# Optimization experiments

Measured on AMD Instinct MI355X. Metric: run time of the kernel, lower is better.

The kernel has to match this reference:

```python
import jax, jax.numpy as jnp
import numpy as np

N, E = 50000, 500000
IN, C, CE_IN = 128, 64, 16   # raw node dim, mid_channel, raw edge dim
L = 3                        # num_layers: layer0 = bare conv, layers 1..2 = res+ blocks
LN_EPS = 1e-5


def layer_norm(x, g, b):
    mu = x.mean(-1, keepdims=True)
    var = ((x - mu) ** 2).mean(-1, keepdims=True)
    return (x - mu) * jax.lax.rsqrt(var + LN_EPS) * g + b


def sage_conv(x, e, src, dst, W1, b1, W2, b2, Wr, t):
    """SAGEConvV2 with softmax aggregation. Returns (node_out, per-edge messages)."""
    # message: lin_l(cat([x_i, x_j, edge_attr])) ; x_i = dst (target), x_j = src (source)
    m_in = jnp.concatenate([x[dst], x[src], e], axis=-1)          # [E, 2C+Ce]
    m = jax.nn.relu(m_in @ W1 + b1) @ W2 + b2                      # [E, C]
    # scatter_softmax(m * t, dst) per feature channel
    logits = m * t
    seg_max = jax.ops.segment_max(logits, dst, num_segments=N)    # [N, C]
    w = jnp.exp(logits - seg_max[dst])
    w = w / jax.ops.segment_sum(w, dst, num_segments=N)[dst]
    out = jax.ops.segment_sum(m * w, dst, num_segments=N)         # [N, C]
    out = out + x @ Wr                                             # root weight (no bias)
    return out, m


def setup_inputs() -> dict:
    key = jax.random.key(0)
    ks = jax.random.split(key, 18)
    f32 = jnp.float32

    def w(k, shape, fan_in):
        return (jax.random.normal(k, shape, f32) / np.sqrt(fan_in)).astype(f32)

    inp = {
        "x": jax.random.normal(ks[0], (N, IN), f32),
        "edge_index": jax.random.randint(ks[1], (2, E), 0, N, dtype=jnp.int64),
        "edge_attr": jax.random.normal(ks[2], (E, CE_IN), f32),
        # encoders
        "node_W": w(ks[3], (IN, C), IN),
        "node_b": jnp.zeros((C,), f32),
        "edge_W": w(ks[4], (CE_IN, C), CE_IN),
        "edge_b": jnp.zeros((C,), f32),
        # stacked conv params (L convs, identical shapes)
        "conv_W1": w(ks[5], (L, 3 * C, 2 * C), 3 * C),
        "conv_b1": jnp.zeros((L, 2 * C), f32),
        "conv_W2": w(ks[6], (L, 2 * C, C), 2 * C),
        "conv_b2": jnp.zeros((L, C), f32),
        "conv_Wr": w(ks[7], (L, C, C), C),
        "conv_t": jnp.ones((L,), f32),
        # layer norms: ln_g[0]/ln_b[0] used as the final output norm, 1..2 inside res+ blocks
        "ln_g": jnp.ones((L, C), f32),
        "ln_b": jnp.zeros((L, C), f32),
        "eln_g": jnp.ones((L - 1, C), f32),
        "eln_b": jnp.zeros((L - 1, C), f32),
    }
    return inp


def reference(x, edge_index, edge_attr, node_W, node_b, edge_W, edge_b,
              conv_W1, conv_b1, conv_W2, conv_b2, conv_Wr, conv_t,
              ln_g, ln_b, eln_g, eln_b):
    src, dst = edge_index[0], edge_index[1]
    h = x @ node_W + node_b                    # node encoder
    e = edge_attr @ edge_W + edge_b            # edge encoder
    # first layer: bare conv
    h, e = sage_conv(h, e, src, dst, conv_W1[0], conv_b1[0], conv_W2[0],
                     conv_b2[0], conv_Wr[0], conv_t[0])
    # res+ blocks (dropout is identity in eval mode)
    for i in range(1, L):
        hn = jax.nn.relu(layer_norm(h, ln_g[i], ln_b[i]))
        en = layer_norm(e, eln_g[i - 1], eln_b[i - 1])
        dh, m = sage_conv(hn, en, src, dst, conv_W1[i], conv_b1[i], conv_W2[i],
                          conv_b2[i], conv_Wr[i], conv_t[i])
        h = h + dh
        e = e + m
    # final norm + act (uses layer-0 norm params, as in the canonical DeeperGCN example)
    return jax.nn.relu(layer_norm(h, ln_g[0], ln_b[0]))
```

## Files before the change

### kernel.cpp

```cpp
#include <hip/hip_runtime.h>

typedef unsigned short u16;
typedef unsigned int u32;
typedef __attribute__((ext_vector_type(8))) short short8;
typedef __attribute__((ext_vector_type(4))) float floatx4;

#define LN_EPS 1e-5f

__device__ __forceinline__ float bf2f(u16 u) {
    union { u32 i; float f; } v; v.i = ((u32)u) << 16; return v.f;
}
__device__ __forceinline__ u16 f2bf(float f) {
    union { u32 i; float f; } v; v.f = f;
    u32 x = v.i;
    return (u16)((x + 0x7fffu + ((x >> 16) & 1u)) >> 16);
}
__device__ __forceinline__ int clampi(int v, int lo, int hi) {
    return v < lo ? lo : (v > hi ? hi : v);
}

__device__ __forceinline__ void g2lds16(const void* g, void* l) {
    __builtin_amdgcn_global_load_lds(
        (__attribute__((address_space(1))) const u32*)g,
        (__attribute__((address_space(3))) u32*)l, 16, 0, 0);
}

__global__ void k_fill(float* __restrict__ out, int nel, float val) {
    int i = blockIdx.x * blockDim.x + threadIdx.x;
    if (i < nel) out[i] = val;
}

__global__ void k_pre0(const int* __restrict__ ei, int E, int* __restrict__ flag,
                       int* __restrict__ deg, int n,
                       const float* __restrict__ W1, const float* __restrict__ W2,
                       const float* __restrict__ Wr, const float* __restrict__ nW,
                       u16* __restrict__ W1s, u16* __restrict__ W2s,
                       u16* __restrict__ Wrs, u16* __restrict__ nWs) {
    int t = threadIdx.x;
    if (blockIdx.x == 0) {
        __shared__ int any;
        if (t == 0) any = 0;
        __syncthreads();
        int lim = (E < 4096) ? E : 4096;
        int v = 0;
        for (int i = t; i < lim; i += 256) v |= ei[2 * i + 1];
        if (v) atomicOr(&any, 1);
        __syncthreads();
        if (t == 0) flag[0] = (any == 0) ? 1 : 0;
    }
    int i = blockIdx.x * 256 + t;
    if (i < n) deg[i] = 0;
    if (i < 3 * 24576) {
        int l = i / 24576, rem = i % 24576;
        int k = rem / 128, c = rem % 128;
        int kt = k >> 5, q = (k >> 3) & 3, j = k & 7;
        W1s[l * 24576 + ((kt * 4 + q) * 128 + c) * 8 + j] = f2bf(W1[i]);
    }
    if (i < 3 * 8192) {
        int l = i / 8192, rem = i % 8192;
        int k = rem / 64, c = rem % 64;
        int kt = k >> 5, q = (k >> 3) & 3, j = k & 7;
        W2s[l * 8192 + ((kt * 4 + q) * 64 + c) * 8 + j] = f2bf(W2[i]);
    }
    if (i < 3 * 4096) {
        int l = i / 4096, rem = i % 4096;
        int k = rem / 64, c = rem % 64;
        int kt = k >> 5, q = (k >> 3) & 3, j = k & 7;
        Wrs[l * 4096 + ((kt * 4 + q) * 64 + c) * 8 + j] = f2bf(Wr[i]);
    }
    if (i < 8192) {
        int k = i / 64, c = i % 64;
        int kt = k >> 5, q = (k >> 3) & 3, j = k & 7;
        nWs[((kt * 4 + q) * 64 + c) * 8 + j] = f2bf(nW[i]);
    }
}

__global__ void k_hist(const int* __restrict__ ei, const int* __restrict__ flag,
                       int* __restrict__ deg, int E, int n) {
    int e = blockIdx.x * blockDim.x + threadIdx.x;
    if (e < E) {
        int d = flag[0] ? ei[2 * ((size_t)E + e)] : ei[(size_t)E + e];
        atomicAdd(&deg[clampi(d, 0, n - 1)], 1);
    }
}

__global__ void k_scan1(const int* __restrict__ deg, int* __restrict__ offs,
                        int* __restrict__ bsum, int n) {
    __shared__ int s[256];
    int t = threadIdx.x;
    int i = blockIdx.x * 256 + t;
    int v = (i < n) ? deg[i] : 0;
    s[t] = v; __syncthreads();
    for (int off = 1; off < 256; off <<= 1) {
        int x = (t >= off) ? s[t - off] : 0;
        __syncthreads();
        s[t] += x;
        __syncthreads();
    }
    if (i < n) offs[i] = s[t] - v;
    if (t == 255) bsum[blockIdx.x] = s[255];
}

__global__ void k_scan23(int* __restrict__ offs, const int* __restrict__ bsum,
                         int* __restrict__ cursor, int n, int E, int nb) {
    __shared__ int s[256];
    int t = threadIdx.x;
    int v = (t < nb) ? bsum[t] : 0;
    s[t] = v; __syncthreads();
    for (int off = 1; off < 256; off <<= 1) {
        int x = (t >= off) ? s[t - off] : 0;
        __syncthreads();
        s[t] += x;
        __syncthreads();
    }
    int excl = s[blockIdx.x] - bsum[blockIdx.x];
    int i = blockIdx.x * 256 + t;
    if (i < n) {
        int val = offs[i] + excl;
        offs[i] = val;
        cursor[i] = val;
    }
    if (i == 0) offs[n] = E;
}

__global__ void k_scatter(const int* __restrict__ ei, const int* __restrict__ flag,
                          int* __restrict__ cursor,
                          int* __restrict__ perm, int* __restrict__ srcs,
                          int* __restrict__ dsts, int E, int n) {
    int e = blockIdx.x * blockDim.x + threadIdx.x;
    if (e < E) {
        int sv, dv;
        if (flag[0]) {
            sv = ei[2 * (size_t)e];
            dv = ei[2 * ((size_t)E + e)];
        } else {
            sv = ei[e];
            dv = ei[(size_t)E + e];
        }
        sv = clampi(sv, 0, n - 1);
        dv = clampi(dv, 0, n - 1);
        int p = clampi(atomicAdd(&cursor[dv], 1), 0, E - 1);
        perm[p] = e;
        srcs[p] = sv;
        dsts[p] = dv;
    }
}

#define HSTR 136

__global__ __launch_bounds__(512) void k_enc(
    const float* __restrict__ x, const u16* __restrict__ nWs, const float* __restrict__ nbias,
    const u16* __restrict__ Wrs0,
    float* __restrict__ h, u16* __restrict__ hn, int n,
    const float* __restrict__ ea, const int* __restrict__ perm,
    const float* __restrict__ eW, const float* __restrict__ ebias,
    u16* __restrict__ e_s, int E, int RB) {
    __shared__ __align__(16) short sA[8 * 16 * HSTR];
    int t = threadIdx.x;
    if ((int)blockIdx.x < RB) {
        int w = t >> 6, l = t & 63, q = l >> 4, ml = l & 15;
        int wbase = blockIdx.x * 128 + w * 16;
        int rin = wbase + ml;
        int rr = (rin < n) ? rin : 0;
        const float* xr = x + (size_t)rr * 128;
        short8 a[4];
#pragma unroll
        for (int kt = 0; kt < 4; kt++) {
            float4 f0 = *((const float4*)(xr + kt * 32 + q * 8));
            float4 f1 = *((const float4*)(xr + kt * 32 + q * 8 + 4));
            a[kt][0] = (short)f2bf(f0.x); a[kt][1] = (short)f2bf(f0.y);
            a[kt][2] = (short)f2bf(f0.z); a[kt][3] = (short)f2bf(f0.w);
            a[kt][4] = (short)f2bf(f1.x); a[kt][5] = (short)f2bf(f1.y);
            a[kt][6] = (short)f2bf(f1.z); a[kt][7] = (short)f2bf(f1.w);
        }
        float bc[4];
#pragma unroll
        for (int nt = 0; nt < 4; nt++) bc[nt] = nbias[nt * 16 + ml];
        floatx4 acc[4];
#pragma unroll
        for (int nt = 0; nt < 4; nt++) acc[nt] = floatx4{0.f, 0.f, 0.f, 0.f};
#pragma unroll
        for (int kt = 0; kt < 4; kt++) {
#pragma unroll
            for (int nt = 0; nt < 4; nt++) {
                short8 bf = *((const short8*)(nWs + (size_t)((kt * 4 + q) * 64 + nt * 16 + ml) * 8));
                acc[nt] = __builtin_amdgcn_mfma_f32_16x16x32_bf16(a[kt], bf, acc[nt], 0, 0, 0);
            }
        }
        short* arena = sA + w * 16 * HSTR;
#pragma unroll
        for (int nt = 0; nt < 4; nt++) {
#pragma unroll
            for (int r2 = 0; r2 < 4; r2++) {
                int pos = wbase + q * 4 + r2;
                float v = acc[nt][r2] + bc[nt];
                u16 bv = f2bf(v);
                arena[(q * 4 + r2) * HSTR + nt * 16 + ml] = (short)bv;
                if (pos < n) hn[(size_t)pos * 64 + nt * 16 + ml] = bv;
            }
        }
        short8 ah[2];
#pragma unroll
        for (int kt = 0; kt < 2; kt++)
            ah[kt] = *((const short8*)(arena + ml * HSTR + kt * 32 + q * 8));
        floatx4 acc2[4];
#pragma unroll
        for (int nt = 0; nt < 4; nt++) acc2[nt] = floatx4{0.f, 0.f, 0.f, 0.f};
#pragma unroll
        for (int kt = 0; kt < 2; kt++) {
#pragma unroll
            for (int nt = 0; nt < 4; nt++) {
                short8 bf = *((const short8*)(Wrs0 + (size_t)((kt * 4 + q) * 64 + nt * 16 + ml) * 8));
                acc2[nt] = __builtin_amdgcn_mfma_f32_16x16x32_bf16(ah[kt], bf, acc2[nt], 0, 0, 0);
            }
        }
#pragma unroll
        for (int nt = 0; nt < 4; nt++) {
#pragma unroll
            for (int r2 = 0; r2 < 4; r2++) {
                int pos = wbase + q * 4 + r2;
                if (pos < n) h[(size_t)pos * 64 + nt * 16 + ml] = acc2[nt][r2];
            }
        }
    } else {
        float4* sW4 = (float4*)sA;
        if (t < 256) sW4[t] = ((const float4*)eW)[t];
        __syncthreads();
        int gid = (blockIdx.x - RB) * 512 + t;
        int eidx = gid >> 2, qq = gid & 3;
        if (eidx >= E) return;
        int e = perm[eidx];
        const float4* row4 = (const float4*)(ea + (size_t)e * 16);
        float4 r4[4];
        r4[0] = row4[0]; r4[1] = row4[1]; r4[2] = row4[2]; r4[3] = row4[3];
        const float* row = (const float*)r4;
        float4 acc[4];
#pragma unroll
        for (int j = 0; j < 4; j++) acc[j] = ((const float4*)ebias)[qq * 4 + j];
#pragma unroll
        for (int k = 0; k < 16; k++) {
            float rv = row[k];
#pragma unroll
            for (int j = 0; j < 4; j++) {
                float4 wv = sW4[k * 16 + qq * 4 + j];
                acc[j].x += rv * wv.x; acc[j].y += rv * wv.y;
                acc[j].z += rv * wv.z; acc[j].w += rv * wv.w;
            }
        }
        u32 pk[8];
#pragma unroll
        for (int j = 0; j < 4; j++) {
            pk[2 * j]     = (u32)f2bf(acc[j].x) | ((u32)f2bf(acc[j].y) << 16);
            pk[2 * j + 1] = (u32)f2bf(acc[j].z) | ((u32)f2bf(acc[j].w) << 16);
        }
        uint4* outp = (uint4*)(e_s + (size_t)eidx * 64 + qq * 16);
        outp[0] = make_uint4(pk[0], pk[1], pk[2], pk[3]);
        outp[1] = make_uint4(pk[4], pk[5], pk[6], pk[7]);
    }
}

#define TILE 256
__global__ __launch_bounds__(512, 4) void k_mlp(
    const u16* __restrict__ hn, const u16* __restrict__ e_s,
    const u16* __restrict__ e_s2,
    const int* __restrict__ dsts, const int* __restrict__ srcs,
    const u16* __restrict__ W1s, const float* __restrict__ b1,
    const u16* __restrict__ W2s, const float* __restrict__ b2,
    const float* __restrict__ elng, const float* __restrict__ elnb,
    int ln_edge, u16* __restrict__ m_out, int E,
    const u16* __restrict__ Wrs, float* __restrict__ h, int do_root, int nn) {
    __shared__ __align__(16) short sW2L[8192];
    __shared__ __align__(16) short sShared[24576];

    int t = threadIdx.x;
    int w = t >> 6, l = t & 63, q = l >> 4, ml = l & 15;
    int base = blockIdx.x * TILE + w * 32;
    int pos0 = base + ml;
    int pos1 = base + 16 + ml;
    bool act0 = pos0 < E, act1 = pos1 < E;
    int pp0 = act0 ? pos0 : 0, pp1 = act1 ? pos1 : 0;
    int dn0 = act0 ? dsts[pos0] : 0;
    int sn0 = act0 ? srcs[pos0] : 0;
    int dn1 = act1 ? dsts[pos1] : 0;
    int sn1 = act1 ? srcs[pos1] : 0;

    {
#pragma unroll
        for (int j = 0; j < 6; j++)
            g2lds16((const char*)W1s + (size_t)(t + j * 512) * 16,
                    (char*)sShared + (size_t)(t + j * 512) * 16);
#pragma unroll
        for (int j = 0; j < 2; j++)
            g2lds16((const char*)W2s + (size_t)(t + j * 512) * 16,
                    (char*)sW2L + (size_t)(t + j * 512) * 16);
    }

    short8 a0[6], a1[6];
    a0[0] = *(const short8*)(hn + (size_t)dn0 * 64 + q * 8);
    a0[1] = *(const short8*)(hn + (size_t)dn0 * 64 + 32 + q * 8);
    a0[2] = *(const short8*)(hn + (size_t)sn0 * 64 + q * 8);
    a0[3] = *(const short8*)(hn + (size_t)sn0 * 64 + 32 + q * 8);
    a1[0] = *(const short8*)(hn + (size_t)dn1 * 64 + q * 8);
    a1[1] = *(const short8*)(hn + (size_t)dn1 * 64 + 32 + q * 8);
    a1[2] = *(const short8*)(hn + (size_t)sn1 * 64 + q * 8);
    a1[3] = *(const short8*)(hn + (size_t)sn1 * 64 + 32 + q * 8);
    short8 e00 = *(const short8*)(e_s + (size_t)pp0 * 64 + q * 8);
    short8 e01 = *(const short8*)(e_s + (size_t)pp0 * 64 + 32 + q * 8);
    short8 e10 = *(const short8*)(e_s + (size_t)pp1 * 64 + q * 8);
    short8 e11 = *(const short8*)(e_s + (size_t)pp1 * 64 + 32 + q * 8);
    short8 f00, f01, f10, f11;
    bool has2 = (e_s2 != nullptr);
    if (has2) {
        f00 = *(const short8*)(e_s2 + (size_t)pp0 * 64 + q * 8);
        f01 = *(const short8*)(e_s2 + (size_t)pp0 * 64 + 32 + q * 8);
        f10 = *(const short8*)(e_s2 + (size_t)pp1 * 64 + q * 8);
        f11 = *(const short8*)(e_s2 + (size_t)pp1 * 64 + 32 + q * 8);
    }

    if (ln_edge) {
        {
            float ev[16];
            float sm = 0.f, sq = 0.f;
#pragma unroll
            for (int i = 0; i < 8; i++) {
                float f0 = bf2f((u16)e00[i]);
                float f1 = bf2f((u16)e01[i]);
                if (has2) { f0 += bf2f((u16)f00[i]); f1 += bf2f((u16)f01[i]); }
                ev[i] = f0; ev[8 + i] = f1;
                sm += f0 + f1; sq += f0 * f0 + f1 * f1;
            }
            sm += __shfl_xor(sm, 16); sm += __shfl_xor(sm, 32);
            sq += __shfl_xor(sq, 16); sq += __shfl_xor(sq, 32);
            float mu = sm * (1.f / 64.f);
            float var = sq * (1.f / 64.f) - mu * mu;
            float inv = rsqrtf(fmaxf(var, 0.f) + LN_EPS);
#pragma unroll
            for (int i = 0; i < 8; i++) {
                int c0 = q * 8 + i, c1 = 32 + q * 8 + i;
                a0[4][i] = (short)f2bf((ev[i] - mu) * inv * elng[c0] + elnb[c0]);
                a0[5][i] = (short)f2bf((ev[8 + i] - mu) * inv * elng[c1] + elnb[c1]);
            }
        }
        {
            float ev[16];
            float sm = 0.f, sq = 0.f;
#pragma unroll
            for (int i = 0; i < 8; i++) {
                float f0 = bf2f((u16)e10[i]);
                float f1 = bf2f((u16)e11[i]);
                if (has2) { f0 += bf2f((u16)f10[i]); f1 += bf2f((u16)f11[i]); }
                ev[i] = f0; ev[8 + i] = f1;
                sm += f0 + f1; sq += f0 * f0 + f1 * f1;
            }
            sm += __shfl_xor(sm, 16); sm += __shfl_xor(sm, 32);
            sq += __shfl_xor(sq, 16); sq += __shfl_xor(sq, 32);
            float mu = sm * (1.f / 64.f);
            float var = sq * (1.f / 64.f) - mu * mu;
            float inv = rsqrtf(fmaxf(var, 0.f) + LN_EPS);
#pragma unroll
            for (int i = 0; i < 8; i++) {
                int c0 = q * 8 + i, c1 = 32 + q * 8 + i;
                a1[4][i] = (short)f2bf((ev[i] - mu) * inv * elng[c0] + elnb[c0]);
                a1[5][i] = (short)f2bf((ev[8 + i] - mu) * inv * elng[c1] + elnb[c1]);
            }
        }
    } else {
        a0[4] = e00; a0[5] = e01;
        a1[4] = e10; a1[5] = e11;
    }

    __syncthreads();

    floatx4 acc0[8], acc1[8];
#pragma unroll
    for (int nt = 0; nt < 8; nt++) {
        acc0[nt] = floatx4{0.f, 0.f, 0.f, 0.f};
        acc1[nt] = floatx4{0.f, 0.f, 0.f, 0.f};
    }
#pragma unroll
    for (int kt = 0; kt < 6; kt++) {
#pragma unroll
        for (int nt = 0; nt < 8; nt++) {
            short8 bf = *((const short8*)(sShared + ((kt * 4 + q) * 128 + nt * 16 + ml) * 8));
            acc0[nt] = __builtin_amdgcn_mfma_f32_16x16x32_bf16(a0[kt], bf, acc0[nt], 0, 0, 0);
            acc1[nt] = __builtin_amdgcn_mfma_f32_16x16x32_bf16(a1[kt], bf, acc1[nt], 0, 0, 0);
        }
    }

    __syncthreads();

    float b1c[8], b2c[4];
#pragma unroll
    for (int nt = 0; nt < 8; nt++) b1c[nt] = b1[nt * 16 + ml];
#pragma unroll
    for (int nt = 0; nt < 4; nt++) b2c[nt] = b2[nt * 16 + ml];

    short* arena = sShared + w * 16 * HSTR;

#pragma unroll
    for (int nt = 0; nt < 8; nt++) {
#pragma unroll
        for (int r2 = 0; r2 < 4; r2++) {
            float v = fmaxf(acc0[nt][r2] + b1c[nt], 0.f);
            ((u16*)arena)[(q * 4 + r2) * HSTR + nt * 16 + ml] = f2bf(v);
        }
    }
    short8 ah0[4];
#pragma unroll
    for (int kt = 0; kt < 4; kt++)
        ah0[kt] = *((const short8*)(arena + ml * HSTR + kt * 32 + q * 8));

#pragma unroll
    for (int nt = 0; nt < 8; nt++) {
#pragma unroll
        for (int r2 = 0; r2 < 4; r2++) {
            float v = fmaxf(acc1[nt][r2] + b1c[nt], 0.f);
            ((u16*)arena)[(q * 4 + r2) * HSTR + nt * 16 + ml] = f2bf(v);
        }
    }
    short8 ah1[4];
#pragma unroll
    for (int kt = 0; kt < 4; kt++)
        ah1[kt] = *((const short8*)(arena + ml * HSTR + kt * 32 + q * 8));

    floatx4 c20[4], c21[4];
#pragma unroll
    for (int nt = 0; nt < 4; nt++) {
        c20[nt] = floatx4{0.f, 0.f, 0.f, 0.f};
        c21[nt] = floatx4{0.f, 0.f, 0.f, 0.f};
    }
#pragma unroll
    for (int kt = 0; kt < 4; kt++) {
#pragma unroll
        for (int nt = 0; nt < 4; nt++) {
            short8 bf = *((const short8*)(sW2L + ((kt * 4 + q) * 64 + nt * 16 + ml) * 8));
            c20[nt] = __builtin_amdgcn_mfma_f32_16x16x32_bf16(ah0[kt], bf, c20[nt], 0, 0, 0);
            c21[nt] = __builtin_amdgcn_mfma_f32_16x16x32_bf16(ah1[kt], bf, c21[nt], 0, 0, 0);
        }
    }

#pragma unroll
    for (int nt = 0; nt < 4; nt++) {
#pragma unroll
        for (int r2 = 0; r2 < 4; r2++) {
            ((u16*)arena)[(q * 4 + r2) * HSTR + nt * 16 + ml] = f2bf(c20[nt][r2] + b2c[nt]);
        }
    }
    {
        short8 m0 = *((const short8*)(arena + ml * HSTR + q * 16));
        short8 m1 = *((const short8*)(arena + ml * HSTR + q * 16 + 8));
        if (act0) {
            *((short8*)(m_out + (size_t)pos0 * 64 + q * 16)) = m0;
            *((short8*)(m_out + (size_t)pos0 * 64 + q * 16 + 8)) = m1;
        }
    }
#pragma unroll
    for (int nt = 0; nt < 4; nt++) {
#pragma unroll
        for (int r2 = 0; r2 < 4; r2++) {
            ((u16*)arena)[(q * 4 + r2) * HSTR + nt * 16 + ml] = f2bf(c21[nt][r2] + b2c[nt]);
        }
    }
    {
        short8 m0 = *((const short8*)(arena + ml * HSTR + q * 16));
        short8 m1 = *((const short8*)(arena + ml * HSTR + q * 16 + 8));
        if (act1) {
            *((short8*)(m_out + (size_t)pos1 * 64 + q * 16)) = m0;
            *((short8*)(m_out + (size_t)pos1 * 64 + q * 16 + 8)) = m1;
        }
    }

    if (do_root && blockIdx.x < ((nn + 127) >> 7)) {
        __syncthreads();
        int nbase = blockIdx.x * 128;
        {
            int r = t >> 2, s = t & 3;
            int pos = nbase + r;
            int g2 = r >> 4, mm = r & 15;
            short* grp = sW2L + g2 * 1024;
            bool ract = pos < nn;
            uint4 z4 = make_uint4(0, 0, 0, 0);
            const uint4* pd = (const uint4*)(hn + (size_t)(ract ? pos : 0) * 64);
            uint4 d0 = ract ? pd[2 * s] : z4;
            uint4 d1 = ract ? pd[2 * s + 1] : z4;
            int ch = (s >> 1) * 4 + (s & 1) * 2;
            *((uint4*)(grp + ch * 128 + mm * 8)) = d0;
            *((uint4*)(grp + (ch + 1) * 128 + mm * 8)) = d1;
        }
        __syncthreads();
        short* rA = sW2L + w * 1024;
        floatx4 racc[4];
#pragma unroll
        for (int nt = 0; nt < 4; nt++) racc[nt] = floatx4{0.f, 0.f, 0.f, 0.f};
#pragma unroll
        for (int kt = 0; kt < 2; kt++) {
            short8 aa = *((const short8*)(rA + (kt * 4 + q) * 128 + ml * 8));
#pragma unroll
            for (int nt = 0; nt < 4; nt++) {
                short8 bf = *((const short8*)(Wrs + (size_t)((kt * 4 + q) * 64 + nt * 16 + ml) * 8));
                racc[nt] = __builtin_amdgcn_mfma_f32_16x16x32_bf16(aa, bf, racc[nt], 0, 0, 0);
            }
        }
#pragma unroll
        for (int nt = 0; nt < 4; nt++) {
#pragma unroll
            for (int r2 = 0; r2 < 4; r2++) {
                int pos = nbase + w * 16 + q * 4 + r2;
                if (pos < nn) {
                    size_t idx = (size_t)pos * 64 + nt * 16 + ml;
                    h[idx] += racc[nt][r2];
                }
            }
        }
    }
}

__global__ __launch_bounds__(256) void k_agg2(
    const u16* __restrict__ m_s, float* __restrict__ h,
    const int* __restrict__ offs, const float* __restrict__ tptr, int tidx,
    const float* __restrict__ g, const float* __restrict__ b,
    u16* __restrict__ hn_out, float* __restrict__ f32_out,
    int write_h, int n, int E) {
    int t = threadIdx.x, wid = t >> 6, lane = t & 63;
    float tv = tptr[tidx];
    float gc = g[lane], bc = b[lane];
    for (int node = blockIdx.x * 4 + wid; node < n; node += gridDim.x * 4) {
        int p0 = clampi(offs[node], 0, E);
        int p1 = clampi(offs[node + 1], p0, E);
        float hv = h[(size_t)node * 64 + lane];
        float M = -1e30f, D = 0.f, S = 0.f;
        for (int p = p0; p < p1; p += 8) {
            int cnt = p1 - p;
            float mv[8], lg[8];
#pragma unroll
            for (int j = 0; j < 8; j++) {
                int idx = (j < cnt) ? (p + j) : (p1 - 1);
                mv[j] = bf2f(m_s[(size_t)idx * 64 + lane]);
                lg[j] = (j < cnt) ? mv[j] * tv : -1e30f;
            }
            float Mc = fmaxf(fmaxf(fmaxf(lg[0], lg[1]), fmaxf(lg[2], lg[3])),
                             fmaxf(fmaxf(lg[4], lg[5]), fmaxf(lg[6], lg[7])));
            float e0 = __expf(lg[0] - Mc), e1 = __expf(lg[1] - Mc);
            float e2 = __expf(lg[2] - Mc), e3 = __expf(lg[3] - Mc);
            float e4 = __expf(lg[4] - Mc), e5 = __expf(lg[5] - Mc);
            float e6 = __expf(lg[6] - Mc), e7 = __expf(lg[7] - Mc);
            float Dc = ((e0 + e1) + (e2 + e3)) + ((e4 + e5) + (e6 + e7));
            float Sc = ((mv[0] * e0 + mv[1] * e1) + (mv[2] * e2 + mv[3] * e3)) +
                       ((mv[4] * e4 + mv[5] * e5) + (mv[6] * e6 + mv[7] * e7));
            float Mn = fmaxf(M, Mc);
            float xa = __expf(M - Mn), xb = __expf(Mc - Mn);
            D = D * xa + Dc * xb;
            S = S * xa + Sc * xb;
            M = Mn;
        }
        if (p1 > p0) hv += S / D;
        if (write_h) h[(size_t)node * 64 + lane] = hv;
        float s = hv;
#pragma unroll
        for (int o = 32; o > 0; o >>= 1) s += __shfl_xor(s, o);
        float mu = s * (1.f / 64.f);
        float d = hv - mu;
        float s2 = d * d;
#pragma unroll
        for (int o = 32; o > 0; o >>= 1) s2 += __shfl_xor(s2, o);
        float inv = rsqrtf(s2 * (1.f / 64.f) + LN_EPS);
        float r = fmaxf(d * inv * gc + bc, 0.f);
        if (hn_out) hn_out[(size_t)node * 64 + lane] = f2bf(r);
        else        f32_out[(size_t)node * 64 + lane] = r;
    }
}

extern "C" void kernel_launch(void* const* d_in, const int* in_sizes, int n_in,
                              void* d_out, int out_size, void* d_ws, size_t ws_size,
                              hipStream_t stream) {
    float* outp = (float*)d_out;
    int FB = (out_size + 255) / 256;

    if (n_in != 17) {
        k_fill<<<FB, 256, 0, stream>>>(outp, out_size, 3.0f);
        return;
    }

    const float* x    = (const float*)d_in[0];
    const int*   ei   = (const int*)d_in[1];
    const float* ea   = (const float*)d_in[2];
    const float* nW   = (const float*)d_in[3];
    const float* nb   = (const float*)d_in[4];
    const float* eW   = (const float*)d_in[5];
    const float* eb   = (const float*)d_in[6];
    const float* cW1  = (const float*)d_in[7];
    const float* cb1  = (const float*)d_in[8];
    const float* cW2  = (const float*)d_in[9];
    const float* cb2  = (const float*)d_in[10];
    const float* cWr  = (const float*)d_in[11];
    const float* ct   = (const float*)d_in[12];
    const float* lng  = (const float*)d_in[13];
    const float* lnb  = (const float*)d_in[14];
    const float* elng = (const float*)d_in[15];
    const float* elnb = (const float*)d_in[16];

    const int n = in_sizes[0] / 128;
    const int E = in_sizes[2] / 16;

    char* ws = (char*)d_ws;
    size_t o = 0;
    auto alloc = [&](size_t bytes) -> void* {
        void* p = ws + o;
        o += (bytes + 255) & ~(size_t)255;
        return p;
    };
    int*   flag   = (int*)alloc(256);
    int*   deg    = (int*)alloc((size_t)n * 4);
    int*   offs   = (int*)alloc((size_t)(n + 1) * 4);
    int*   cursor = (int*)alloc((size_t)n * 4);
    int*   bsum   = (int*)alloc(256 * 4);
    int*   perm   = (int*)alloc((size_t)E * 4);
    int*   srcs   = (int*)alloc((size_t)E * 4);
    int*   dsts   = (int*)alloc((size_t)E * 4);
    float* h      = (float*)alloc((size_t)n * 64 * 4);
    u16*   hn     = (u16*)alloc((size_t)n * 64 * 2);
    u16*   bufA   = (u16*)alloc((size_t)E * 64 * 2);
    u16*   bufB   = (u16*)alloc((size_t)E * 64 * 2);
    u16*   W1s    = (u16*)alloc((size_t)3 * 24576 * 2);
    u16*   W2s    = (u16*)alloc((size_t)3 * 8192 * 2);
    u16*   Wrs    = (u16*)alloc((size_t)3 * 4096 * 2);
    u16*   nWs    = (u16*)alloc((size_t)8192 * 2);

    if (o > ws_size) {
        k_fill<<<FB, 256, 0, stream>>>(outp, out_size, 2.0f);
        return;
    }

    int SB = (n + 255) / 256;
    int PB = (3 * 24576 + 255) / 256;
    if (SB > PB) PB = SB;
    k_pre0<<<PB, 256, 0, stream>>>(ei, E, flag, deg, n,
                                   cW1, cW2, cWr, nW, W1s, W2s, Wrs, nWs);
    k_hist<<<(E + 255) / 256, 256, 0, stream>>>(ei, flag, deg, E, n);
    k_scan1<<<SB, 256, 0, stream>>>(deg, offs, bsum, n);
    k_scan23<<<SB, 256, 0, stream>>>(offs, bsum, cursor, n, E, SB);
    k_scatter<<<(E + 255) / 256, 256, 0, stream>>>(ei, flag, cursor, perm, srcs, dsts, E, n);

    int RB = (n + 127) / 128;
    int EB2 = (E * 4 + 511) / 512;
    k_enc<<<RB + EB2, 512, 0, stream>>>(x, nWs, nb, Wrs, h, hn, n,
                                        ea, perm, eW, eb, bufA, E, RB);

    int MB = (E + TILE - 1) / TILE;
    int AB = (n + 3) / 4;

    const u16* mlp_in[3]  = { bufA, bufB, bufB };
    const u16* mlp_in2[3] = { nullptr, nullptr, bufA };
    u16*       mlp_out[3] = { bufB, bufA, bufA };

    for (int i = 0; i < 3; i++) {
        k_mlp<<<MB, 512, 0, stream>>>(
            hn, mlp_in[i], mlp_in2[i], dsts, srcs,
            W1s + (size_t)i * 24576, cb1 + (size_t)i * 128,
            W2s + (size_t)i * 8192, cb2 + (size_t)i * 64,
            elng + (size_t)((i > 0) ? (i - 1) : 0) * 64,
            elnb + (size_t)((i > 0) ? (i - 1) : 0) * 64,
            (i > 0) ? 1 : 0, mlp_out[i], E,
            Wrs + (size_t)i * 4096, h, (i > 0) ? 1 : 0, n);
        if (i < 2) {
            k_agg2<<<AB, 256, 0, stream>>>(mlp_out[i], h, offs, ct, i,
                                           lng + (size_t)(i + 1) * 64, lnb + (size_t)(i + 1) * 64,
                                           hn, nullptr, 1, n, E);
        } else {
            k_agg2<<<AB, 256, 0, stream>>>(mlp_out[i], h, offs, ct, i,
                                           lng, lnb,
                                           nullptr, outp, 0, n, E);
        }
    }
}
```

Before: 485.0 us.

## Fuse CSR preprocessing kernels into one cooperative kernel with grid syncs

Merges the weight-swizzle, degree histogram, two-level scan and edge scatter kernels into a single cooperative launch of 512 blocks that uses grid-stride loops and grid.sync() between phases. The aim is to remove four kernel launch gaps. In exchange, the histogram and scatter phases run with fewer threads in flight, and the grid-wide barriers add their own cost.

```diff
diff --git a/kernel.cpp b/kernel.cpp
--- a/kernel.cpp
+++ b/kernel.cpp
@@ -1,4 +1,7 @@
 #include <hip/hip_runtime.h>
+#include <hip/hip_cooperative_groups.h>
+
+namespace cg = cooperative_groups;
 
 typedef unsigned short u16;
 typedef unsigned int u32;
@@ -30,13 +33,23 @@
     if (i < nel) out[i] = val;
 }
 
-__global__ void k_pre0(const int* __restrict__ ei, int E, int* __restrict__ flag,
-                       int* __restrict__ deg, int n,
-                       const float* __restrict__ W1, const float* __restrict__ W2,
-                       const float* __restrict__ Wr, const float* __restrict__ nW,
-                       u16* __restrict__ W1s, u16* __restrict__ W2s,
-                       u16* __restrict__ Wrs, u16* __restrict__ nWs) {
+__global__ __launch_bounds__(256) void k_pre(
+    const int* __restrict__ ei, int E, int* __restrict__ flag,
+    int* __restrict__ deg, int n,
+    const float* __restrict__ W1, const float* __restrict__ W2,
+    const float* __restrict__ Wr, const float* __restrict__ nW,
+    u16* __restrict__ W1s, u16* __restrict__ W2s,
+    u16* __restrict__ Wrs, u16* __restrict__ nWs,
+    int* __restrict__ offs, int* __restrict__ bsum, int* __restrict__ cursor,
+    int* __restrict__ perm, int* __restrict__ srcs, int* __restrict__ dsts,
+    int SB) {
+    cg::grid_group grid = cg::this_grid();
+    __shared__ int s[256];
     int t = threadIdx.x;
+    int nb = gridDim.x;
+    int gstep = nb * 256;
+    int gid0 = blockIdx.x * 256 + t;
+
     if (blockIdx.x == 0) {
         __shared__ int any;
         if (t == 0) any = 0;
@@ -48,101 +61,98 @@
         __syncthreads();
         if (t == 0) flag[0] = (any == 0) ? 1 : 0;
     }
-    int i = blockIdx.x * 256 + t;
-    if (i < n) deg[i] = 0;
-    if (i < 3 * 24576) {
-        int l = i / 24576, rem = i % 24576;
-        int k = rem / 128, c = rem % 128;
-        int kt = k >> 5, q = (k >> 3) & 3, j = k & 7;
-        W1s[l * 24576 + ((kt * 4 + q) * 128 + c) * 8 + j] = f2bf(W1[i]);
-    }
-    if (i < 3 * 8192) {
-        int l = i / 8192, rem = i % 8192;
-        int k = rem / 64, c = rem % 64;
-        int kt = k >> 5, q = (k >> 3) & 3, j = k & 7;
-        W2s[l * 8192 + ((kt * 4 + q) * 64 + c) * 8 + j] = f2bf(W2[i]);
-    }
-    if (i < 3 * 4096) {
-        int l = i / 4096, rem = i % 4096;
-        int k = rem / 64, c = rem % 64;
-        int kt = k >> 5, q = (k >> 3) & 3, j = k & 7;
-        Wrs[l * 4096 + ((kt * 4 + q) * 64 + c) * 8 + j] = f2bf(Wr[i]);
-    }
-    if (i < 8192) {
-        int k = i / 64, c = i % 64;
-        int kt = k >> 5, q = (k >> 3) & 3, j = k & 7;
-        nWs[((kt * 4 + q) * 64 + c) * 8 + j] = f2bf(nW[i]);
-    }
-}
-
-__global__ void k_hist(const int* __restrict__ ei, const int* __restrict__ flag,
-                       int* __restrict__ deg, int E, int n) {
-    int e = blockIdx.x * blockDim.x + threadIdx.x;
-    if (e < E) {
-        int d = flag[0] ? ei[2 * ((size_t)E + e)] : ei[(size_t)E + e];
-        atomicAdd(&deg[clampi(d, 0, n - 1)], 1);
-    }
-}
-
-__global__ void k_scan1(const int* __restrict__ deg, int* __restrict__ offs,
-                        int* __restrict__ bsum, int n) {
-    __shared__ int s[256];
-    int t = threadIdx.x;
-    int i = blockIdx.x * 256 + t;
-    int v = (i < n) ? deg[i] : 0;
-    s[t] = v; __syncthreads();
-    for (int off = 1; off < 256; off <<= 1) {
-        int x = (t >= off) ? s[t - off] : 0;
+    for (int i = gid0; i < n; i += gstep) deg[i] = 0;
+    for (int i = gid0; i < 3 * 24576; i += gstep) {
+        {
+            int l = i / 24576, rem = i % 24576;
+            int k = rem / 128, c = rem % 128;
+            int kt = k >> 5, q = (k >> 3) & 3, j = k & 7;
+            W1s[l * 24576 + ((kt * 4 + q) * 128 + c) * 8 + j] = f2bf(W1[i]);
+        }
+        if (i < 3 * 8192) {
+            int l = i / 8192, rem = i % 8192;
+            int k = rem / 64, c = rem % 64;
+            int kt = k >> 5, q = (k >> 3) & 3, j = k & 7;
+            W2s[l * 8192 + ((kt * 4 + q) * 64 + c) * 8 + j] = f2bf(W2[i]);
+        }
+        if (i < 3 * 4096) {
+            int l = i / 4096, rem = i % 4096;
+            int k = rem / 64, c = rem % 64;
+            int kt = k >> 5, q = (k >> 3) & 3, j = k & 7;
+            Wrs[l * 4096 + ((kt * 4 + q) * 64 + c) * 8 + j] = f2bf(Wr[i]);
+        }
+        if (i < 8192) {
+            int k = i / 64, c = i % 64;
+            int kt = k >> 5, q = (k >> 3) & 3, j = k & 7;
+            nWs[((kt * 4 + q) * 64 + c) * 8 + j] = f2bf(nW[i]);
+        }
+    }
+    grid.sync();
+
+    {
+        int f = flag[0];
+        for (int e = gid0; e < E; e += gstep) {
+            int d = f ? ei[2 * ((size_t)E + e)] : ei[(size_t)E + e];
+            atomicAdd(&deg[clampi(d, 0, n - 1)], 1);
+        }
+    }
+    grid.sync();
+
+    for (int seg = blockIdx.x; seg < SB; seg += nb) {
+        int i = seg * 256 + t;
+        int v = (i < n) ? deg[i] : 0;
+        s[t] = v; __syncthreads();
+        for (int off = 1; off < 256; off <<= 1) {
+            int x = (t >= off) ? s[t - off] : 0;
+            __syncthreads();
+            s[t] += x;
+            __syncthreads();
+        }
+        if (i < n) offs[i] = s[t] - v;
+        if (t == 255) bsum[seg] = s[255];
         __syncthreads();
-        s[t] += x;
+    }
+    grid.sync();
+
+    for (int seg = blockIdx.x; seg < SB; seg += nb) {
+        int v = (t < SB) ? bsum[t] : 0;
+        s[t] = v; __syncthreads();
+        for (int off = 1; off < 256; off <<= 1) {
+            int x = (t >= off) ? s[t - off] : 0;
+            __syncthreads();
+            s[t] += x;
+            __syncthreads();
+        }
+        int excl = s[seg] - bsum[seg];
+        int i = seg * 256 + t;
+        if (i < n) {
+            int val = offs[i] + excl;
+            offs[i] = val;
+            cursor[i] = val;
+        }
+        if (i == 0) offs[n] = E;
         __syncthreads();
     }
-    if (i < n) offs[i] = s[t] - v;
-    if (t == 255) bsum[blockIdx.x] = s[255];
-}
-
-__global__ void k_scan23(int* __restrict__ offs, const int* __restrict__ bsum,
-                         int* __restrict__ cursor, int n, int E, int nb) {
-    __shared__ int s[256];
-    int t = threadIdx.x;
-    int v = (t < nb) ? bsum[t] : 0;
-    s[t] = v; __syncthreads();
-    for (int off = 1; off < 256; off <<= 1) {
-        int x = (t >= off) ? s[t - off] : 0;
-        __syncthreads();
-        s[t] += x;
-        __syncthreads();
-    }
-    int excl = s[blockIdx.x] - bsum[blockIdx.x];
-    int i = blockIdx.x * 256 + t;
-    if (i < n) {
-        int val = offs[i] + excl;
-        offs[i] = val;
-        cursor[i] = val;
-    }
-    if (i == 0) offs[n] = E;
-}
-
-__global__ void k_scatter(const int* __restrict__ ei, const int* __restrict__ flag,
-                          int* __restrict__ cursor,
-                          int* __restrict__ perm, int* __restrict__ srcs,
-                          int* __restrict__ dsts, int E, int n) {
-    int e = blockIdx.x * blockDim.x + threadIdx.x;
-    if (e < E) {
-        int sv, dv;
-        if (flag[0]) {
-            sv = ei[2 * (size_t)e];
-            dv = ei[2 * ((size_t)E + e)];
-        } else {
-            sv = ei[e];
-            dv = ei[(size_t)E + e];
-        }
-        sv = clampi(sv, 0, n - 1);
-        dv = clampi(dv, 0, n - 1);
-        int p = clampi(atomicAdd(&cursor[dv], 1), 0, E - 1);
-        perm[p] = e;
-        srcs[p] = sv;
-        dsts[p] = dv;
+    grid.sync();
+
+    {
+        int f = flag[0];
+        for (int e = gid0; e < E; e += gstep) {
+            int sv, dv;
+            if (f) {
+                sv = ei[2 * (size_t)e];
+                dv = ei[2 * ((size_t)E + e)];
+            } else {
+                sv = ei[e];
+                dv = ei[(size_t)E + e];
+            }
+            sv = clampi(sv, 0, n - 1);
+            dv = clampi(dv, 0, n - 1);
+            int p = clampi(atomicAdd(&cursor[dv], 1), 0, E - 1);
+            perm[p] = e;
+            srcs[p] = sv;
+            dsts[p] = dv;
+        }
     }
 }
 
@@ -632,14 +642,19 @@
     }
 
     int SB = (n + 255) / 256;
-    int PB = (3 * 24576 + 255) / 256;
-    if (SB > PB) PB = SB;
-    k_pre0<<<PB, 256, 0, stream>>>(ei, E, flag, deg, n,
-                                   cW1, cW2, cWr, nW, W1s, W2s, Wrs, nWs);
-    k_hist<<<(E + 255) / 256, 256, 0, stream>>>(ei, flag, deg, E, n);
-    k_scan1<<<SB, 256, 0, stream>>>(deg, offs, bsum, n);
-    k_scan23<<<SB, 256, 0, stream>>>(offs, bsum, cursor, n, E, SB);
-    k_scatter<<<(E + 255) / 256, 256, 0, stream>>>(ei, flag, cursor, perm, srcs, dsts, E, n);
+
+    {
+        int E_ = E, n_ = n, SB_ = SB;
+        void* args[] = {
+            (void*)&ei, (void*)&E_, (void*)&flag, (void*)&deg, (void*)&n_,
+            (void*)&cW1, (void*)&cW2, (void*)&cWr, (void*)&nW,
+            (void*)&W1s, (void*)&W2s, (void*)&Wrs, (void*)&nWs,
+            (void*)&offs, (void*)&bsum, (void*)&cursor,
+            (void*)&perm, (void*)&srcs, (void*)&dsts, (void*)&SB_
+        };
+        hipLaunchCooperativeKernel((const void*)k_pre, dim3(512), dim3(256),
+                                   args, 0, stream);
+    }
 
     int RB = (n + 127) / 128;
     int EB2 = (E * 4 + 511) / 512;
```

Result: slower. 750.1 us (+54.7%).
